# Optimization experiments

Measured on AMD Instinct MI355X. Metric: run time of the kernel, lower is better.

## Reference

```python
import jax, jax.numpy as jnp
import numpy as np

D = 512; H = 8; DH = D // H; DFF = 4 * D; INNER = 2 * D; K = 31
B = 8; S = 1024
EPS = 1e-5


def layer_norm(x, g, b):
    m = jnp.mean(x, axis=-1, keepdims=True)
    v = jnp.mean(jnp.square(x - m), axis=-1, keepdims=True)
    return (x - m) * jax.lax.rsqrt(v + EPS) * g + b


def setup_inputs() -> dict:
    key = jax.random.key(0)
    ks = iter(jax.random.split(key, 32))
    w = lambda *s: jax.random.normal(next(ks), s, dtype=jnp.float32) * 0.02
    d = {
        "x": jax.random.normal(next(ks), (B, S, D), dtype=jnp.float32),
        # FF module 1
        "ln1_g": jnp.ones((D,)), "ln1_b": jnp.zeros((D,)),
        "ff1_w1": w(DFF, D), "ff1_b1": jnp.zeros((DFF,)),
        "ff1_w2": w(D, DFF), "ff1_b2": jnp.zeros((D,)),
        # attention
        "lna_g": jnp.ones((D,)), "lna_b": jnp.zeros((D,)),
        "qkv_w": w(3 * D, D), "qkv_b": jnp.zeros((3 * D,)),
        "out_w": w(D, D), "out_b": jnp.zeros((D,)),
        # conv module
        "lnc_g": jnp.ones((D,)), "lnc_b": jnp.zeros((D,)),
        "pw1_w": w(INNER, D), "pw1_b": jnp.zeros((INNER,)),
        "dw_w": w(D, 1, K), "dw_b": jnp.zeros((D,)),
        "bn_g": jnp.ones((D,)), "bn_b": jnp.zeros((D,)),
        "bn_mean": jnp.zeros((D,)), "bn_var": jnp.ones((D,)),
        "pw2_w": w(D, D), "pw2_b": jnp.zeros((D,)),
        # FF module 2
        "ln2_g": jnp.ones((D,)), "ln2_b": jnp.zeros((D,)),
        "ff2_w1": w(DFF, D), "ff2_b1": jnp.zeros((DFF,)),
        "ff2_w2": w(D, DFF), "ff2_b2": jnp.zeros((D,)),
        # final layer norm
        "lnf_g": jnp.ones((D,)), "lnf_b": jnp.zeros((D,)),
    }
    return d


def _ff(x, g, b, w1, b1, w2, b2):
    h = layer_norm(x, g, b)
    h = jax.nn.silu(h @ w1.T + b1)
    h = h @ w2.T + b2
    return h + x  # FeedForwardModule adds its own residual


def _attn(x, g, b, qkv_w, qkv_b, out_w, out_b):
    h = layer_norm(x, g, b)
    qkv = (h @ qkv_w.T + qkv_b).reshape(B, S, 3, H, DH)
    q, k, v = qkv[:, :, 0], qkv[:, :, 1], qkv[:, :, 2]  # [B,S,H,DH]
    scores = jnp.einsum('bqhd,bkhd->bhqk', q, k) / np.sqrt(DH).astype(np.float32)
    probs = jax.nn.softmax(scores, axis=-1)
    ctx = jnp.einsum('bhqk,bkhd->bqhd', probs, v).reshape(B, S, D)
    return ctx @ out_w.T + out_b


def _conv(x, g, b, pw1_w, pw1_b, dw_w, dw_b, bn_g, bn_b, bn_mean, bn_var, pw2_w, pw2_b):
    h = layer_norm(x, g, b)
    y = h @ pw1_w.T + pw1_b                      # [B,S,2D] pointwise conv1
    a, gate = jnp.split(y, 2, axis=-1)           # GLU along channel dim
    y = a * jax.nn.sigmoid(gate)                 # [B,S,D]
    y = y.transpose(0, 2, 1)                     # [B,D,S]
    y = jax.lax.conv_general_dilated(
        y, dw_w, window_strides=(1,), padding=((K // 2, K // 2),),
        dimension_numbers=('NCH', 'OIH', 'NCH'), feature_group_count=D)
    y = y + dw_b[None, :, None]
    y = (y - bn_mean[None, :, None]) * jax.lax.rsqrt(bn_var + EPS)[None, :, None]
    y = y * bn_g[None, :, None] + bn_b[None, :, None]
    y = jax.nn.silu(y)
    y = y.transpose(0, 2, 1)                     # [B,S,D]
    y = y @ pw2_w.T + pw2_b
    return y + x  # ConvModule adds its own residual


def reference(x, ln1_g, ln1_b, ff1_w1, ff1_b1, ff1_w2, ff1_b2,
              lna_g, lna_b, qkv_w, qkv_b, out_w, out_b,
              lnc_g, lnc_b, pw1_w, pw1_b, dw_w, dw_b,
              bn_g, bn_b, bn_mean, bn_var, pw2_w, pw2_b,
              ln2_g, ln2_b, ff2_w1, ff2_b1, ff2_w2, ff2_b2,
              lnf_g, lnf_b):
    x = x + 0.5 * _ff(x, ln1_g, ln1_b, ff1_w1, ff1_b1, ff1_w2, ff1_b2)
    x = x + _attn(x, lna_g, lna_b, qkv_w, qkv_b, out_w, out_b)
    x = x + _conv(x, lnc_g, lnc_b, pw1_w, pw1_b, dw_w, dw_b,
                  bn_g, bn_b, bn_mean, bn_var, pw2_w, pw2_b)
    x = x + 0.5 * _ff(x, ln2_g, ln2_b, ff2_w1, ff2_b1, ff2_w2, ff2_b2)
    return layer_norm(x, lnf_g, lnf_b)
```

## Files before the change

kernel.cpp:

```cpp
#include <hip/hip_runtime.h>
#include <hip/hip_bf16.h>

typedef __attribute__((ext_vector_type(8))) short bf16x8;
typedef __attribute__((ext_vector_type(4))) float f32x4;

#define NTOK 8192
#define SEQ  1024
#define NH   8

__device__ __forceinline__ float bfs2f(short s) {
  union { unsigned u; float f; } x; x.u = ((unsigned)(unsigned short)s) << 16; return x.f;
}
__device__ __forceinline__ short f2bfs(float f) {
  __hip_bfloat16 h = __float2bfloat16(f);
  return *reinterpret_cast<short*>(&h);
}
__device__ __forceinline__ float bfp2f(const __hip_bfloat16* p) {
  return bfs2f(*reinterpret_cast<const short*>(p));
}

__device__ __forceinline__ void gld16(const void* g, void* l) {
  __builtin_amdgcn_global_load_lds(
      (__attribute__((address_space(1))) void*)const_cast<void*>(g),
      (__attribute__((address_space(3))) void*)l, 16, 0, 0);
}

struct WSeg { const float* src; unsigned dst_off; unsigned nvec; };
struct WPack { WSeg s[8]; };

__global__ __launch_bounds__(256) void cast_wall_kernel(WPack p,
                                                        __hip_bfloat16* __restrict__ dst) {
  unsigned v = blockIdx.x * 256 + threadIdx.x;
#pragma unroll
  for (int t = 0; t < 8; ++t) {
    if (v < p.s[t].nvec) {
      const float* s = p.s[t].src + (size_t)v * 8;
      f32x4 a = *reinterpret_cast<const f32x4*>(s);
      f32x4 b = *reinterpret_cast<const f32x4*>(s + 4);
      bf16x8 o;
#pragma unroll
      for (int j = 0; j < 4; ++j) { o[j] = f2bfs(a[j]); o[4 + j] = f2bfs(b[j]); }
      *reinterpret_cast<bf16x8*>(reinterpret_cast<short*>(dst) +
                                 (size_t)(p.s[t].dst_off + v) * 8) = o;
      return;
    }
    v -= p.s[t].nvec;
  }
}

__global__ __launch_bounds__(256) void cast_dww_kernel(const float* __restrict__ src,
                                                       __hip_bfloat16* __restrict__ dst) {
  for (int k = 0; k < 31; ++k)
    for (int c = threadIdx.x; c < 512; c += 256)
      dst[k * 512 + c] = __float2bfloat16(src[c * 31 + k]);
}

struct PtrPack { const void* p[23]; };

__global__ __launch_bounds__(256) void cast_small_kernel(PtrPack pk,
                                                         __hip_bfloat16* __restrict__ dst) {
  constexpr int sizes[23] = {512, 512, 2048, 512, 512, 512, 1536, 512, 512, 512, 1024, 512,
                             512, 512, 512, 512, 512, 512, 512, 2048, 512, 512, 512};
  int off = 0;
  for (int t = 0; t < 23; ++t) {
    const int n = sizes[t];
    for (int i = threadIdx.x; i < n; i += 256)
      dst[off + i] = __float2bfloat16(((const float*)pk.p[t])[i]);
    off += n;
  }
}

__global__ void ws_bad_kernel(float* __restrict__ out) {
  if (threadIdx.x == 0) out[0] = 5000.f;
}

__global__ __launch_bounds__(256) void ln_kernel(const float* __restrict__ in,
                                                 const __hip_bfloat16* __restrict__ g,
                                                 const __hip_bfloat16* __restrict__ b,
                                                 __hip_bfloat16* __restrict__ out) {
  const int wv = threadIdx.x >> 6, ln = threadIdx.x & 63;
  const int row = blockIdx.x * 4 + wv;
  const float* p = in + (size_t)row * 512 + ln * 8;
  float v[8];
  {
    const f32x4* p4 = reinterpret_cast<const f32x4*>(p);
    f32x4 a = p4[0], c = p4[1];
#pragma unroll
    for (int j = 0; j < 4; ++j) { v[j] = a[j]; v[4 + j] = c[j]; }
  }
  float s = 0.f;
#pragma unroll
  for (int j = 0; j < 8; ++j) s += v[j];
  for (int m = 1; m < 64; m <<= 1) s += __shfl_xor(s, m);
  const float mean = s * (1.f / 512.f);
  float q = 0.f;
#pragma unroll
  for (int j = 0; j < 8; ++j) { float d = v[j] - mean; q += d * d; }
  for (int m = 1; m < 64; m <<= 1) q += __shfl_xor(q, m);
  const float rstd = rsqrtf(q * (1.f / 512.f) + 1e-5f);
  bf16x8 gg = *reinterpret_cast<const bf16x8*>(g + ln * 8);
  bf16x8 bb = *reinterpret_cast<const bf16x8*>(b + ln * 8);
  bf16x8 ov;
#pragma unroll
  for (int j = 0; j < 8; ++j)
    ov[j] = f2bfs((v[j] - mean) * rstd * bfs2f(gg[j]) + bfs2f(bb[j]));
  *reinterpret_cast<bf16x8*>(out + (size_t)row * 512 + ln * 8) = ov;
}

__global__ __launch_bounds__(256) void lnf_kernel(const float* __restrict__ in,
                                                  const __hip_bfloat16* __restrict__ g,
                                                  const __hip_bfloat16* __restrict__ b,
                                                  float* __restrict__ out) {
  const int wv = threadIdx.x >> 6, ln = threadIdx.x & 63;
  const int row = blockIdx.x * 4 + wv;
  const float* p = in + (size_t)row * 512 + ln * 8;
  float v[8];
  {
    const f32x4* p4 = reinterpret_cast<const f32x4*>(p);
    f32x4 a = p4[0], c = p4[1];
#pragma unroll
    for (int j = 0; j < 4; ++j) { v[j] = a[j]; v[4 + j] = c[j]; }
  }
  float s = 0.f;
#pragma unroll
  for (int j = 0; j < 8; ++j) s += v[j];
  for (int m = 1; m < 64; m <<= 1) s += __shfl_xor(s, m);
  const float mean = s * (1.f / 512.f);
  float q = 0.f;
#pragma unroll
  for (int j = 0; j < 8; ++j) { float d = v[j] - mean; q += d * d; }
  for (int m = 1; m < 64; m <<= 1) q += __shfl_xor(q, m);
  const float rstd = rsqrtf(q * (1.f / 512.f) + 1e-5f);
  bf16x8 gg = *reinterpret_cast<const bf16x8*>(g + ln * 8);
  bf16x8 bb = *reinterpret_cast<const bf16x8*>(b + ln * 8);
  f32x4 o0, o1;
#pragma unroll
  for (int j = 0; j < 4; ++j) {
    o0[j] = (v[j] - mean) * rstd * bfs2f(gg[j]) + bfs2f(bb[j]);
    o1[j] = (v[4 + j] - mean) * rstd * bfs2f(gg[4 + j]) + bfs2f(bb[4 + j]);
  }
  float* op = out + (size_t)row * 512 + ln * 8;
  *reinterpret_cast<f32x4*>(op) = o0;
  *reinterpret_cast<f32x4*>(op + 4) = o1;
}

template <int EPI>
__global__ __launch_bounds__(256, 3) void gemm_bt(const __hip_bfloat16* __restrict__ A,
                                                  const __hip_bfloat16* __restrict__ W,
                                                  const __hip_bfloat16* __restrict__ bias,
                                                  __hip_bfloat16* __restrict__ outb,
                                                  float* __restrict__ resid,
                                                  int K, int M, float alpha, float beta) {
  __shared__ __align__(16) __hip_bfloat16 As[128 * 64];
  __shared__ __align__(16) __hip_bfloat16 Bs[128 * 64];
  const int tid = threadIdx.x;
  const int wv = tid >> 6, ln = tid & 63;
  const int hi = ln >> 4, lo = ln & 15;
  const int lo7 = lo & 7;
  const int gx = gridDim.x;
  const int nwg = gx * gridDim.y;
  const int t = blockIdx.y * gx + blockIdx.x;
  const int w = (t & 7) * (nwg >> 3) + (t >> 3);
  const int n0 = (w & (gx - 1)) * 128;
  const int m0 = (w / gx) * 128;
  const int wr = wv >> 1, wc = wv & 1;
  const int srow = ln >> 3;
  const int scolz = (((ln & 7) ^ srow) << 3);

  f32x4 acc[4][4] = {};

  for (int k0 = 0; k0 < K; k0 += 64) {
    __syncthreads();
#pragma unroll
    for (int i = 0; i < 4; ++i) {
      const int grp = i * 4 + wv;
      const int row = grp * 8 + srow;
      gld16(A + (size_t)(n0 + row) * K + k0 + scolz, As + grp * 512);
      gld16(W + (size_t)(m0 + row) * K + k0 + scolz, Bs + grp * 512);
    }
    __syncthreads();
#pragma unroll
    for (int kk2 = 0; kk2 < 2; ++kk2) {
      const int g0 = ((kk2 * 4 + hi) ^ lo7) << 3;
      bf16x8 af[4], bfr[4];
#pragma unroll
      for (int r = 0; r < 4; ++r)
        af[r] = *reinterpret_cast<const bf16x8*>(As + (wr * 64 + r * 16 + lo) * 64 + g0);
#pragma unroll
      for (int c = 0; c < 4; ++c)
        bfr[c] = *reinterpret_cast<const bf16x8*>(Bs + (wc * 64 + c * 16 + lo) * 64 + g0);
#pragma unroll
      for (int r = 0; r < 4; ++r)
#pragma unroll
        for (int c = 0; c < 4; ++c)
          acc[r][c] = __builtin_amdgcn_mfma_f32_16x16x32_bf16(af[r], bfr[c], acc[r][c], 0, 0, 0);
    }
  }

#pragma unroll
  for (int r = 0; r < 4; ++r) {
#pragma unroll
    for (int c = 0; c < 4; ++c) {
      const int m = m0 + wc * 64 + c * 16 + lo;
      const float bv = bfp2f(bias + m);
#pragma unroll
      for (int j = 0; j < 4; ++j) {
        const int n = n0 + wr * 64 + r * 16 + hi * 4 + j;
        float v = acc[r][c][j] + bv;
        if constexpr (EPI == 1) v = v / (1.f + __expf(-v));
        if constexpr (EPI <= 1) {
          outb[(size_t)n * M + m] = __float2bfloat16(v);
        } else {
          const size_t idx = (size_t)n * 512 + m;
          resid[idx] = alpha * resid[idx] + beta * v;
        }
      }
    }
  }
}

__global__ __launch_bounds__(256, 4) void gemm64_resid(const __hip_bfloat16* __restrict__ A,
                                                       const __hip_bfloat16* __restrict__ W,
                                                       const __hip_bfloat16* __restrict__ bias,
                                                       const float* __restrict__ rsrc,
                                                       float* __restrict__ resid,
                                                       int K, float alpha, float beta) {
  __shared__ __align__(16) __hip_bfloat16 As[64 * 64];
  __shared__ __align__(16) __hip_bfloat16 Bs[128 * 64];
  const int tid = threadIdx.x;
  const int wv = tid >> 6, ln = tid & 63;
  const int hi = ln >> 4, lo = ln & 15;
  const int lo7 = lo & 7;
  const int gx = gridDim.x;
  const int nwg = gx * gridDim.y;
  const int t = blockIdx.y * gx + blockIdx.x;
  const int w = (t & 7) * (nwg >> 3) + (t >> 3);
  const int n0 = (w & (gx - 1)) * 64;
  const int m0 = (w / gx) * 128;
  const int wr = wv >> 1, wc = wv & 1;
  const int srow = ln >> 3;
  const int scolz = (((ln & 7) ^ srow) << 3);

  f32x4 acc[2][4] = {};

  for (int k0 = 0; k0 < K; k0 += 64) {
    __syncthreads();
#pragma unroll
    for (int i = 0; i < 2; ++i) {
      const int grp = i * 4 + wv;
      gld16(A + (size_t)(n0 + grp * 8 + srow) * K + k0 + scolz, As + grp * 512);
    }
#pragma unroll
    for (int i = 0; i < 4; ++i) {
      const int grp = i * 4 + wv;
      gld16(W + (size_t)(m0 + grp * 8 + srow) * K + k0 + scolz, Bs + grp * 512);
    }
    __syncthreads();
#pragma unroll
    for (int kk2 = 0; kk2 < 2; ++kk2) {
      const int g0 = ((kk2 * 4 + hi) ^ lo7) << 3;
      bf16x8 af[2], bfr[4];
#pragma unroll
      for (int r = 0; r < 2; ++r)
        af[r] = *reinterpret_cast<const bf16x8*>(As + (wr * 32 + r * 16 + lo) * 64 + g0);
#pragma unroll
      for (int c = 0; c < 4; ++c)
        bfr[c] = *reinterpret_cast<const bf16x8*>(Bs + (wc * 64 + c * 16 + lo) * 64 + g0);
#pragma unroll
      for (int r = 0; r < 2; ++r)
#pragma unroll
        for (int c = 0; c < 4; ++c)
          acc[r][c] = __builtin_amdgcn_mfma_f32_16x16x32_bf16(af[r], bfr[c], acc[r][c], 0, 0, 0);
    }
  }

#pragma unroll
  for (int r = 0; r < 2; ++r) {
#pragma unroll
    for (int c = 0; c < 4; ++c) {
      const int m = m0 + wc * 64 + c * 16 + lo;
      const float bv = bfp2f(bias + m);
#pragma unroll
      for (int j = 0; j < 4; ++j) {
        const int n = n0 + wr * 32 + r * 16 + hi * 4 + j;
        const size_t idx = (size_t)n * 512 + m;
        resid[idx] = alpha * rsrc[idx] + beta * (acc[r][c][j] + bv);
      }
    }
  }
}

__global__ __launch_bounds__(256) void vtrans_kernel(const __hip_bfloat16* __restrict__ qkv,
                                                     __hip_bfloat16* __restrict__ vT) {
  __shared__ __hip_bfloat16 tile[64][65];
  const int bh = blockIdx.x;
  const int s0 = blockIdx.y * 64;
  const int b = bh >> 3, h = bh & 7;
  const int c = threadIdx.x & 63;
  const int r4 = threadIdx.x >> 6;
#pragma unroll
  for (int i = 0; i < 16; ++i) {
    const int s = r4 * 16 + i;
    tile[s][c] = qkv[(size_t)(b * 1024 + s0 + s) * 1536 + 1024 + h * 64 + c];
  }
  __syncthreads();
#pragma unroll
  for (int i = 0; i < 16; ++i) {
    const int d = r4 * 16 + i;
    vT[((size_t)bh * 64 + d) * 1024 + s0 + c] = tile[c][d];
  }
}

__global__ __launch_bounds__(256, 2) void attn_kernel(const __hip_bfloat16* __restrict__ qkv,
                                                      const __hip_bfloat16* __restrict__ vT,
                                                      __hip_bfloat16* __restrict__ ctx) {
  __shared__ __align__(16) short Ks[2][64 * 64];
  __shared__ __align__(16) short Vs[2][64 * 64];
  __shared__ __align__(16) short P[4][16][64];
  const int tid = threadIdx.x;
  const int wv = tid >> 6, ln = tid & 63;
  const int hi = ln >> 4, lo = ln & 15;
  const int lo7 = lo & 7;
  const int blk = ((blockIdx.x & 7) << 6) | (blockIdx.x >> 3);
  const int qt = blk & 7, h = (blk >> 3) & 7, b = blk >> 6;
  const int q0 = qt * 128 + wv * 16;

  const int srow8 = ln >> 3;
  const int gsrc = (ln & 7) ^ srow8;

  bf16x8 aq0a, aq1a, aq0b, aq1b;
  {
    const __hip_bfloat16* qpa = qkv + (size_t)(b * SEQ + q0 + lo) * 1536 + h * 64 + hi * 8;
    const __hip_bfloat16* qpb = qpa + (size_t)64 * 1536;
    bf16x8 r0 = *reinterpret_cast<const bf16x8*>(qpa);
    bf16x8 r1 = *reinterpret_cast<const bf16x8*>(qpa + 32);
    bf16x8 r2 = *reinterpret_cast<const bf16x8*>(qpb);
    bf16x8 r3 = *reinterpret_cast<const bf16x8*>(qpb + 32);
#pragma unroll
    for (int j = 0; j < 8; ++j) {
      aq0a[j] = f2bfs(bfs2f(r0[j]) * 0.125f);
      aq1a[j] = f2bfs(bfs2f(r1[j]) * 0.125f);
      aq0b[j] = f2bfs(bfs2f(r2[j]) * 0.125f);
      aq1b[j] = f2bfs(bfs2f(r3[j]) * 0.125f);
    }
  }

  const __hip_bfloat16* kbase = qkv + 512 + h * 64 + (size_t)b * SEQ * 1536;
  const __hip_bfloat16* vbase = vT + (size_t)(b * NH + h) * 64 * 1024;

  f32x4 oaccA[4] = {}, oaccB[4] = {};
  float lrowA[4] = {0.f, 0.f, 0.f, 0.f};
  float lrowB[4] = {0.f, 0.f, 0.f, 0.f};

#pragma unroll
  for (int c = 0; c < 2; ++c) {
    const int r = c * 32 + wv * 8 + srow8;
    gld16(kbase + (size_t)r * 1536 + gsrc * 8, &Ks[0][(c * 32 + wv * 8) * 64]);
    gld16(vbase + (size_t)r * 1024 + gsrc * 8, &Vs[0][(c * 32 + wv * 8) * 64]);
  }
  __syncthreads();

  int cb = 0;
  for (int kt = 0; kt < 16; ++kt) {
    if (kt < 15) {
      const int kb2 = (kt + 1) * 64;
#pragma unroll
      for (int c = 0; c < 2; ++c) {
        const int r = c * 32 + wv * 8 + srow8;
        gld16(kbase + (size_t)(kb2 + r) * 1536 + gsrc * 8,
              &Ks[cb ^ 1][(c * 32 + wv * 8) * 64]);
        gld16(vbase + (size_t)r * 1024 + kb2 + gsrc * 8,
              &Vs[cb ^ 1][(c * 32 + wv * 8) * 64]);
      }
    }

    bf16x8 bk0[4], bk1[4];
#pragma unroll
    for (int nt = 0; nt < 4; ++nt) {
      const short* kr = &Ks[cb][(nt * 16 + lo) * 64];
      bk0[nt] = *reinterpret_cast<const bf16x8*>(kr + ((hi ^ lo7) << 3));
      bk1[nt] = *reinterpret_cast<const bf16x8*>(kr + (((hi + 4) ^ lo7) << 3));
    }
    f32x4 scA[4] = {}, scB[4] = {};
#pragma unroll
    for (int nt = 0; nt < 4; ++nt) {
      scA[nt] = __builtin_amdgcn_mfma_f32_16x16x32_bf16(aq0a, bk0[nt], scA[nt], 0, 0, 0);
      scA[nt] = __builtin_amdgcn_mfma_f32_16x16x32_bf16(aq1a, bk1[nt], scA[nt], 0, 0, 0);
      scB[nt] = __builtin_amdgcn_mfma_f32_16x16x32_bf16(aq0b, bk0[nt], scB[nt], 0, 0, 0);
      scB[nt] = __builtin_amdgcn_mfma_f32_16x16x32_bf16(aq1b, bk1[nt], scB[nt], 0, 0, 0);
    }

    bf16x8 bv0[4], bv1[4];
#pragma unroll
    for (int dt = 0; dt < 4; ++dt) {
      const short* vr = &Vs[cb][(dt * 16 + lo) * 64];
      bv0[dt] = *reinterpret_cast<const bf16x8*>(vr + ((hi ^ lo7) << 3));
      bv1[dt] = *reinterpret_cast<const bf16x8*>(vr + (((hi + 4) ^ lo7) << 3));
    }

#pragma unroll
    for (int j = 0; j < 4; ++j) {
      const int prow = hi * 4 + j;
      const int pswz = (prow & 7) << 3;
#pragma unroll
      for (int nt = 0; nt < 4; ++nt) {
        const float p = __expf(scA[nt][j]);
        P[wv][prow][(nt * 16 + lo) ^ pswz] = f2bfs(p);
        lrowA[j] += p;
      }
    }
    asm volatile("" ::: "memory");
    {
      const short* pr = &P[wv][lo][0];
      bf16x8 ap0 = *reinterpret_cast<const bf16x8*>(pr + ((hi ^ lo7) << 3));
      bf16x8 ap1 = *reinterpret_cast<const bf16x8*>(pr + (((hi + 4) ^ lo7) << 3));
#pragma unroll
      for (int dt = 0; dt < 4; ++dt) {
        oaccA[dt] = __builtin_amdgcn_mfma_f32_16x16x32_bf16(ap0, bv0[dt], oaccA[dt], 0, 0, 0);
        oaccA[dt] = __builtin_amdgcn_mfma_f32_16x16x32_bf16(ap1, bv1[dt], oaccA[dt], 0, 0, 0);
      }
    }
    asm volatile("" ::: "memory");

#pragma unroll
    for (int j = 0; j < 4; ++j) {
      const int prow = hi * 4 + j;
      const int pswz = (prow & 7) << 3;
#pragma unroll
      for (int nt = 0; nt < 4; ++nt) {
        const float p = __expf(scB[nt][j]);
        P[wv][prow][(nt * 16 + lo) ^ pswz] = f2bfs(p);
        lrowB[j] += p;
      }
    }
    asm volatile("" ::: "memory");
    {
      const short* pr = &P[wv][lo][0];
      bf16x8 ap0 = *reinterpret_cast<const bf16x8*>(pr + ((hi ^ lo7) << 3));
      bf16x8 ap1 = *reinterpret_cast<const bf16x8*>(pr + (((hi + 4) ^ lo7) << 3));
#pragma unroll
      for (int dt = 0; dt < 4; ++dt) {
        oaccB[dt] = __builtin_amdgcn_mfma_f32_16x16x32_bf16(ap0, bv0[dt], oaccB[dt], 0, 0, 0);
        oaccB[dt] = __builtin_amdgcn_mfma_f32_16x16x32_bf16(ap1, bv1[dt], oaccB[dt], 0, 0, 0);
      }
    }
    __syncthreads();
    cb ^= 1;
  }

#pragma unroll
  for (int j = 0; j < 4; ++j) {
    float sa = lrowA[j], sb = lrowB[j];
    sa += __shfl_xor(sa, 1); sb += __shfl_xor(sb, 1);
    sa += __shfl_xor(sa, 2); sb += __shfl_xor(sb, 2);
    sa += __shfl_xor(sa, 4); sb += __shfl_xor(sb, 4);
    sa += __shfl_xor(sa, 8); sb += __shfl_xor(sb, 8);
    lrowA[j] = sa; lrowB[j] = sb;
  }

#pragma unroll
  for (int dt = 0; dt < 4; ++dt)
#pragma unroll
    for (int j = 0; j < 4; ++j) {
      const int d = h * 64 + dt * 16 + lo;
      const int na = b * SEQ + q0 + hi * 4 + j;
      ctx[(size_t)na * 512 + d] = __float2bfloat16(oaccA[dt][j] / lrowA[j]);
      const int nb = na + 64;
      ctx[(size_t)nb * 512 + d] = __float2bfloat16(oaccB[dt][j] / lrowB[j]);
    }
}

__global__ __launch_bounds__(256) void glu8_kernel(const __hip_bfloat16* __restrict__ y,
                                                   __hip_bfloat16* __restrict__ o) {
  const int i = blockIdx.x * 256 + threadIdx.x;
  const int c8 = i & 63;
  const int n = i >> 6;
  const short* yp = reinterpret_cast<const short*>(y) + (size_t)n * 1024 + c8 * 8;
  bf16x8 a = *reinterpret_cast<const bf16x8*>(yp);
  bf16x8 g = *reinterpret_cast<const bf16x8*>(yp + 512);
  bf16x8 ov;
#pragma unroll
  for (int j = 0; j < 8; ++j) {
    const float av = bfs2f(a[j]);
    const float gv = bfs2f(g[j]);
    ov[j] = f2bfs(av / (1.f + __expf(-gv)));
  }
  *reinterpret_cast<bf16x8*>(reinterpret_cast<short*>(o) + (size_t)n * 512 + c8 * 8) = ov;
}

__global__ __launch_bounds__(256) void dwconv8_kernel(const __hip_bfloat16* __restrict__ cin,
                                                      const __hip_bfloat16* __restrict__ wkT,
                                                      const __hip_bfloat16* __restrict__ cb,
                                                      const __hip_bfloat16* __restrict__ bng,
                                                      const __hip_bfloat16* __restrict__ bnb,
                                                      const __hip_bfloat16* __restrict__ bnm,
                                                      const __hip_bfloat16* __restrict__ bnv,
                                                      __hip_bfloat16* __restrict__ outp) {
  const int i = blockIdx.x * 256 + threadIdx.x;
  const int c8 = i & 63;
  const int n = i >> 6;
  const int t = n & 1023;
  const int base = n - t;
  const int co = c8 * 8;

  float acc[8];
  {
    bf16x8 bv = *reinterpret_cast<const bf16x8*>(cb + co);
#pragma unroll
    for (int j = 0; j < 8; ++j) acc[j] = bfs2f(bv[j]);
  }
  const int k0 = (t >= 15) ? 0 : (15 - t);
  const int k1 = (t <= SEQ - 16) ? 31 : (SEQ - 1 - t + 16);
  const short* cin_s = reinterpret_cast<const short*>(cin);
  const short* wk_s = reinterpret_cast<const short*>(wkT);
  for (int k = k0; k < k1; ++k) {
    const int ts = t + k - 15;
    bf16x8 xv = *reinterpret_cast<const bf16x8*>(cin_s + (((size_t)(base + ts)) << 9) + co);
    bf16x8 wv = *reinterpret_cast<const bf16x8*>(wk_s + k * 512 + co);
#pragma unroll
    for (int j = 0; j < 8; ++j) acc[j] += bfs2f(xv[j]) * bfs2f(wv[j]);
  }
  bf16x8 g = *reinterpret_cast<const bf16x8*>(bng + co);
  bf16x8 bb = *reinterpret_cast<const bf16x8*>(bnb + co);
  bf16x8 bm = *reinterpret_cast<const bf16x8*>(bnm + co);
  bf16x8 bvv = *reinterpret_cast<const bf16x8*>(bnv + co);
  bf16x8 ov;
#pragma unroll
  for (int j = 0; j < 8; ++j) {
    const float scl = bfs2f(g[j]) * rsqrtf(bfs2f(bvv[j]) + 1e-5f);
    float v = (acc[j] - bfs2f(bm[j])) * scl + bfs2f(bb[j]);
    v = v / (1.f + __expf(-v));
    ov[j] = f2bfs(v);
  }
  *reinterpret_cast<bf16x8*>(reinterpret_cast<short*>(outp) + ((size_t)n << 9) + co) = ov;
}

extern "C" void kernel_launch(void* const* d_in, const int* in_sizes, int n_in,
                              void* d_out, int out_size, void* d_ws, size_t ws_size,
                              hipStream_t stream) {
  float* out = (float*)d_out;
  if (ws_size < ((size_t)80 << 20)) {
    ws_bad_kernel<<<1, 64, 0, stream>>>(out);
    return;
  }

  const float* x = (const float*)d_in[0];

  char* ws = (char*)d_ws;
  float*          xs = (float*)ws;
  __hip_bfloat16* t0 = (__hip_bfloat16*)(ws + ((size_t)16 << 20));
  __hip_bfloat16* t1 = (__hip_bfloat16*)(ws + ((size_t)24 << 20));
  __hip_bfloat16* t2 = (__hip_bfloat16*)(ws + ((size_t)56 << 20));
  __hip_bfloat16* wc = (__hip_bfloat16*)(ws + ((size_t)64 << 20));
  __hip_bfloat16* vT = t1 + (size_t)NTOK * 1536;

  __hip_bfloat16* wc_ff1_w1 = wc + 0;
  __hip_bfloat16* wc_ff1_w2 = wc + 1048576;
  __hip_bfloat16* wc_qkv_w  = wc + 2097152;
  __hip_bfloat16* wc_out_w  = wc + 2883584;
  __hip_bfloat16* wc_pw1_w  = wc + 3145728;
  __hip_bfloat16* wc_pw2_w  = wc + 3670016;
  __hip_bfloat16* wc_ff2_w1 = wc + 3932160;
  __hip_bfloat16* wc_ff2_w2 = wc + 4980736;
  __hip_bfloat16* wc_dwT    = wc + 6029312;
  __hip_bfloat16* sm        = wc + 6045184;
  __hip_bfloat16* c_ln1_g = sm + 0,     *c_ln1_b = sm + 512,   *c_ff1_b1 = sm + 1024;
  __hip_bfloat16* c_ff1_b2 = sm + 3072, *c_lna_g = sm + 3584,  *c_lna_b = sm + 4096;
  __hip_bfloat16* c_qkv_b = sm + 4608,  *c_out_b = sm + 6144,  *c_lnc_g = sm + 6656;
  __hip_bfloat16* c_lnc_b = sm + 7168,  *c_pw1_b = sm + 7680,  *c_dw_b = sm + 8704;
  __hip_bfloat16* c_bn_g = sm + 9216,   *c_bn_b = sm + 9728,   *c_bn_m = sm + 10240;
  __hip_bfloat16* c_bn_v = sm + 10752,  *c_pw2_b = sm + 11264, *c_ln2_g = sm + 11776;
  __hip_bfloat16* c_ln2_b = sm + 12288, *c_ff2_b1 = sm + 12800, *c_ff2_b2 = sm + 14848;
  __hip_bfloat16* c_lnf_g = sm + 15360, *c_lnf_b = sm + 15872;

  {
    WPack wp;
    wp.s[0] = {(const float*)d_in[3],  0,      131072};
    wp.s[1] = {(const float*)d_in[5],  131072, 131072};
    wp.s[2] = {(const float*)d_in[9],  262144, 98304};
    wp.s[3] = {(const float*)d_in[11], 360448, 32768};
    wp.s[4] = {(const float*)d_in[15], 393216, 65536};
    wp.s[5] = {(const float*)d_in[23], 458752, 32768};
    wp.s[6] = {(const float*)d_in[27], 491520, 131072};
    wp.s[7] = {(const float*)d_in[29], 622592, 131072};
    cast_wall_kernel<<<2944, 256, 0, stream>>>(wp, wc);
  }
  cast_dww_kernel<<<1, 256, 0, stream>>>((const float*)d_in[17], wc_dwT);
  PtrPack pk;
  const int small_idx[23] = {1, 2, 4, 6, 7, 8, 10, 12, 13, 14, 16, 18,
                             19, 20, 21, 22, 24, 25, 26, 28, 30, 31, 32};
  for (int t = 0; t < 23; ++t) pk.p[t] = d_in[small_idx[t]];
  cast_small_kernel<<<1, 256, 0, stream>>>(pk, sm);

  ln_kernel<<<2048, 256, 0, stream>>>(x, c_ln1_g, c_ln1_b, t0);
  gemm_bt<1><<<dim3(64, 16), 256, 0, stream>>>(t0, wc_ff1_w1, c_ff1_b1, t1, nullptr, 512, 2048, 0.f, 0.f);
  gemm64_resid<<<dim3(128, 4), 256, 0, stream>>>(t1, wc_ff1_w2, c_ff1_b2, x, xs, 2048, 1.5f, 0.5f);

  ln_kernel<<<2048, 256, 0, stream>>>(xs, c_lna_g, c_lna_b, t0);
  gemm_bt<0><<<dim3(64, 12), 256, 0, stream>>>(t0, wc_qkv_w, c_qkv_b, t1, nullptr, 512, 1536, 0.f, 0.f);
  vtrans_kernel<<<dim3(64, 16), 256, 0, stream>>>(t1, vT);
  attn_kernel<<<512, 256, 0, stream>>>(t1, vT, t2);
  gemm64_resid<<<dim3(128, 4), 256, 0, stream>>>(t2, wc_out_w, c_out_b, xs, xs, 512, 1.0f, 1.0f);

  ln_kernel<<<2048, 256, 0, stream>>>(xs, c_lnc_g, c_lnc_b, t0);
  gemm_bt<0><<<dim3(64, 8), 256, 0, stream>>>(t0, wc_pw1_w, c_pw1_b, t1, nullptr, 512, 1024, 0.f, 0.f);
  glu8_kernel<<<2048, 256, 0, stream>>>(t1, t2);
  dwconv8_kernel<<<2048, 256, 0, stream>>>(t2, wc_dwT, c_dw_b, c_bn_g, c_bn_b, c_bn_m, c_bn_v, t0);
  gemm64_resid<<<dim3(128, 4), 256, 0, stream>>>(t0, wc_pw2_w, c_pw2_b, xs, xs, 512, 2.0f, 1.0f);

  ln_kernel<<<2048, 256, 0, stream>>>(xs, c_ln2_g, c_ln2_b, t0);
  gemm_bt<1><<<dim3(64, 16), 256, 0, stream>>>(t0, wc_ff2_w1, c_ff2_b1, t1, nullptr, 512, 2048, 0.f, 0.f);
  gemm64_resid<<<dim3(128, 4), 256, 0, stream>>>(t1, wc_ff2_w2, c_ff2_b2, xs, xs, 2048, 1.5f, 0.5f);

  lnf_kernel<<<2048, 256, 0, stream>>>(xs, c_lnf_g, c_lnf_b, out);
}
```

Baseline: 303.3 us.

## Fuse V transpose into QKV GEMM epilogue and keep depthwise conv in fp32

The QKV GEMM gets a new epilogue (EPI==3) that writes the V columns straight into the transposed vT layout as 4-element bf16 vectors, which removes the separate vtrans kernel and its extra read and write of V. Separately, the GLU output and the depthwise conv weights are now stored in fp32 instead of bf16, and the conv loads fp32 vectors. This looks like a precision change that doubles the conv's input traffic. The fused epilogue also writes 8-byte strided stores instead of going through a shared-memory transpose.

New measurement: 319.1 us. +5.2%, slower.

```diff
diff --git a/kernel.cpp b/kernel.cpp
--- a/kernel.cpp
+++ b/kernel.cpp
@@ -2,6 +2,7 @@
 #include <hip/hip_bf16.h>
 
 typedef __attribute__((ext_vector_type(8))) short bf16x8;
+typedef __attribute__((ext_vector_type(4))) short bf16x4;
 typedef __attribute__((ext_vector_type(4))) float f32x4;
 
 #define NTOK 8192
@@ -48,11 +49,11 @@
   }
 }
 
-__global__ __launch_bounds__(256) void cast_dww_kernel(const float* __restrict__ src,
-                                                       __hip_bfloat16* __restrict__ dst) {
+__global__ __launch_bounds__(256) void cast_dwwf_kernel(const float* __restrict__ src,
+                                                        float* __restrict__ dst) {
   for (int k = 0; k < 31; ++k)
     for (int c = threadIdx.x; c < 512; c += 256)
-      dst[k * 512 + c] = __float2bfloat16(src[c * 31 + k]);
+      dst[k * 512 + c] = src[c * 31 + k];
 }
 
 struct PtrPack { const void* p[23]; };
@@ -150,6 +151,7 @@
                                                   const __hip_bfloat16* __restrict__ bias,
                                                   __hip_bfloat16* __restrict__ outb,
                                                   float* __restrict__ resid,
+                                                  __hip_bfloat16* __restrict__ vTout,
                                                   int K, int M, float alpha, float beta) {
   __shared__ __align__(16) __hip_bfloat16 As[128 * 64];
   __shared__ __align__(16) __hip_bfloat16 Bs[128 * 64];
@@ -203,16 +205,29 @@
     for (int c = 0; c < 4; ++c) {
       const int m = m0 + wc * 64 + c * 16 + lo;
       const float bv = bfp2f(bias + m);
+      const int nb = n0 + wr * 64 + r * 16 + hi * 4;
+      if constexpr (EPI == 3) {
+        if (m >= 1024) {
+          const int hd = m - 1024;
+          __hip_bfloat16* vp = vTout +
+              ((size_t)((nb >> 10) * NH + (hd >> 6)) * 64 + (hd & 63)) * 1024 + (nb & 1023);
+          bf16x4 vv;
+#pragma unroll
+          for (int j = 0; j < 4; ++j) vv[j] = f2bfs(acc[r][c][j] + bv);
+          *reinterpret_cast<bf16x4*>(vp) = vv;
+          continue;
+        }
+      }
 #pragma unroll
       for (int j = 0; j < 4; ++j) {
-        const int n = n0 + wr * 64 + r * 16 + hi * 4 + j;
+        const int n = nb + j;
         float v = acc[r][c][j] + bv;
         if constexpr (EPI == 1) v = v / (1.f + __expf(-v));
-        if constexpr (EPI <= 1) {
-          outb[(size_t)n * M + m] = __float2bfloat16(v);
-        } else {
+        if constexpr (EPI == 2) {
           const size_t idx = (size_t)n * 512 + m;
           resid[idx] = alpha * resid[idx] + beta * v;
+        } else {
+          outb[(size_t)n * M + m] = __float2bfloat16(v);
         }
       }
     }
@@ -290,27 +305,6 @@
   }
 }
 
-__global__ __launch_bounds__(256) void vtrans_kernel(const __hip_bfloat16* __restrict__ qkv,
-                                                     __hip_bfloat16* __restrict__ vT) {
-  __shared__ __hip_bfloat16 tile[64][65];
-  const int bh = blockIdx.x;
-  const int s0 = blockIdx.y * 64;
-  const int b = bh >> 3, h = bh & 7;
-  const int c = threadIdx.x & 63;
-  const int r4 = threadIdx.x >> 6;
-#pragma unroll
-  for (int i = 0; i < 16; ++i) {
-    const int s = r4 * 16 + i;
-    tile[s][c] = qkv[(size_t)(b * 1024 + s0 + s) * 1536 + 1024 + h * 64 + c];
-  }
-  __syncthreads();
-#pragma unroll
-  for (int i = 0; i < 16; ++i) {
-    const int d = r4 * 16 + i;
-    vT[((size_t)bh * 64 + d) * 1024 + s0 + c] = tile[c][d];
-  }
-}
-
 __global__ __launch_bounds__(256, 2) void attn_kernel(const __hip_bfloat16* __restrict__ qkv,
                                                       const __hip_bfloat16* __restrict__ vT,
                                                       __hip_bfloat16* __restrict__ ctx) {
@@ -470,32 +464,35 @@
     }
 }
 
-__global__ __launch_bounds__(256) void glu8_kernel(const __hip_bfloat16* __restrict__ y,
-                                                   __hip_bfloat16* __restrict__ o) {
+__global__ __launch_bounds__(256) void glu8f_kernel(const __hip_bfloat16* __restrict__ y,
+                                                    float* __restrict__ o) {
   const int i = blockIdx.x * 256 + threadIdx.x;
   const int c8 = i & 63;
   const int n = i >> 6;
   const short* yp = reinterpret_cast<const short*>(y) + (size_t)n * 1024 + c8 * 8;
   bf16x8 a = *reinterpret_cast<const bf16x8*>(yp);
   bf16x8 g = *reinterpret_cast<const bf16x8*>(yp + 512);
-  bf16x8 ov;
-#pragma unroll
-  for (int j = 0; j < 8; ++j) {
-    const float av = bfs2f(a[j]);
-    const float gv = bfs2f(g[j]);
-    ov[j] = f2bfs(av / (1.f + __expf(-gv)));
-  }
-  *reinterpret_cast<bf16x8*>(reinterpret_cast<short*>(o) + (size_t)n * 512 + c8 * 8) = ov;
-}
-
-__global__ __launch_bounds__(256) void dwconv8_kernel(const __hip_bfloat16* __restrict__ cin,
-                                                      const __hip_bfloat16* __restrict__ wkT,
-                                                      const __hip_bfloat16* __restrict__ cb,
-                                                      const __hip_bfloat16* __restrict__ bng,
-                                                      const __hip_bfloat16* __restrict__ bnb,
-                                                      const __hip_bfloat16* __restrict__ bnm,
-                                                      const __hip_bfloat16* __restrict__ bnv,
-                                                      __hip_bfloat16* __restrict__ outp) {
+  f32x4 o0, o1;
+#pragma unroll
+  for (int j = 0; j < 4; ++j) {
+    const float a0 = bfs2f(a[j]), g0 = bfs2f(g[j]);
+    const float a1 = bfs2f(a[4 + j]), g1 = bfs2f(g[4 + j]);
+    o0[j] = a0 / (1.f + __expf(-g0));
+    o1[j] = a1 / (1.f + __expf(-g1));
+  }
+  float* op = o + (size_t)n * 512 + c8 * 8;
+  *reinterpret_cast<f32x4*>(op) = o0;
+  *reinterpret_cast<f32x4*>(op + 4) = o1;
+}
+
+__global__ __launch_bounds__(256) void dwconv8f_kernel(const float* __restrict__ cin,
+                                                       const float* __restrict__ wkT,
+                                                       const __hip_bfloat16* __restrict__ cb,
+                                                       const __hip_bfloat16* __restrict__ bng,
+                                                       const __hip_bfloat16* __restrict__ bnb,
+                                                       const __hip_bfloat16* __restrict__ bnm,
+                                                       const __hip_bfloat16* __restrict__ bnv,
+                                                       __hip_bfloat16* __restrict__ outp) {
   const int i = blockIdx.x * 256 + threadIdx.x;
   const int c8 = i & 63;
   const int n = i >> 6;
@@ -511,14 +508,19 @@
   }
   const int k0 = (t >= 15) ? 0 : (15 - t);
   const int k1 = (t <= SEQ - 16) ? 31 : (SEQ - 1 - t + 16);
-  const short* cin_s = reinterpret_cast<const short*>(cin);
-  const short* wk_s = reinterpret_cast<const short*>(wkT);
   for (int k = k0; k < k1; ++k) {
     const int ts = t + k - 15;
-    bf16x8 xv = *reinterpret_cast<const bf16x8*>(cin_s + (((size_t)(base + ts)) << 9) + co);
-    bf16x8 wv = *reinterpret_cast<const bf16x8*>(wk_s + k * 512 + co);
-#pragma unroll
-    for (int j = 0; j < 8; ++j) acc[j] += bfs2f(xv[j]) * bfs2f(wv[j]);
+    const float* xp = cin + (((size_t)(base + ts)) << 9) + co;
+    const float* wp = wkT + k * 512 + co;
+    f32x4 x0 = *reinterpret_cast<const f32x4*>(xp);
+    f32x4 x1 = *reinterpret_cast<const f32x4*>(xp + 4);
+    f32x4 w0 = *reinterpret_cast<const f32x4*>(wp);
+    f32x4 w1 = *reinterpret_cast<const f32x4*>(wp + 4);
+#pragma unroll
+    for (int j = 0; j < 4; ++j) {
+      acc[j] += x0[j] * w0[j];
+      acc[4 + j] += x1[j] * w1[j];
+    }
   }
   bf16x8 g = *reinterpret_cast<const bf16x8*>(bng + co);
   bf16x8 bb = *reinterpret_cast<const bf16x8*>(bnb + co);
@@ -547,12 +549,14 @@
   const float* x = (const float*)d_in[0];
 
   char* ws = (char*)d_ws;
-  float*          xs = (float*)ws;
-  __hip_bfloat16* t0 = (__hip_bfloat16*)(ws + ((size_t)16 << 20));
-  __hip_bfloat16* t1 = (__hip_bfloat16*)(ws + ((size_t)24 << 20));
-  __hip_bfloat16* t2 = (__hip_bfloat16*)(ws + ((size_t)56 << 20));
-  __hip_bfloat16* wc = (__hip_bfloat16*)(ws + ((size_t)64 << 20));
-  __hip_bfloat16* vT = t1 + (size_t)NTOK * 1536;
+  float*          xs  = (float*)ws;
+  __hip_bfloat16* t0  = (__hip_bfloat16*)(ws + ((size_t)16 << 20));
+  __hip_bfloat16* t1  = (__hip_bfloat16*)(ws + ((size_t)24 << 20));
+  float*          t2f = (float*)(ws + ((size_t)40 << 20));
+  __hip_bfloat16* t2  = (__hip_bfloat16*)(ws + ((size_t)56 << 20));
+  __hip_bfloat16* wc  = (__hip_bfloat16*)(ws + ((size_t)64 << 20));
+  float*          dwTf = (float*)(ws + ((size_t)78 << 20));
+  __hip_bfloat16* vT  = t1 + (size_t)NTOK * 1536;
 
   __hip_bfloat16* wc_ff1_w1 = wc + 0;
   __hip_bfloat16* wc_ff1_w2 = wc + 1048576;
@@ -562,7 +566,6 @@
   __hip_bfloat16* wc_pw2_w  = wc + 3670016;
   __hip_bfloat16* wc_ff2_w1 = wc + 3932160;
   __hip_bfloat16* wc_ff2_w2 = wc + 4980736;
-  __hip_bfloat16* wc_dwT    = wc + 6029312;
   __hip_bfloat16* sm        = wc + 6045184;
   __hip_bfloat16* c_ln1_g = sm + 0,     *c_ln1_b = sm + 512,   *c_ff1_b1 = sm + 1024;
   __hip_bfloat16* c_ff1_b2 = sm + 3072, *c_lna_g = sm + 3584,  *c_lna_b = sm + 4096;
@@ -585,7 +588,7 @@
     wp.s[7] = {(const float*)d_in[29], 622592, 131072};
     cast_wall_kernel<<<2944, 256, 0, stream>>>(wp, wc);
   }
-  cast_dww_kernel<<<1, 256, 0, stream>>>((const float*)d_in[17], wc_dwT);
+  cast_dwwf_kernel<<<1, 256, 0, stream>>>((const float*)d_in[17], dwTf);
   PtrPack pk;
   const int small_idx[23] = {1, 2, 4, 6, 7, 8, 10, 12, 13, 14, 16, 18,
                              19, 20, 21, 22, 24, 25, 26, 28, 30, 31, 32};
@@ -593,23 +596,22 @@
   cast_small_kernel<<<1, 256, 0, stream>>>(pk, sm);
 
   ln_kernel<<<2048, 256, 0, stream>>>(x, c_ln1_g, c_ln1_b, t0);
-  gemm_bt<1><<<dim3(64, 16), 256, 0, stream>>>(t0, wc_ff1_w1, c_ff1_b1, t1, nullptr, 512, 2048, 0.f, 0.f);
+  gemm_bt<1><<<dim3(64, 16), 256, 0, stream>>>(t0, wc_ff1_w1, c_ff1_b1, t1, nullptr, nullptr, 512, 2048, 0.f, 0.f);
   gemm64_resid<<<dim3(128, 4), 256, 0, stream>>>(t1, wc_ff1_w2, c_ff1_b2, x, xs, 2048, 1.5f, 0.5f);
 
   ln_kernel<<<2048, 256, 0, stream>>>(xs, c_lna_g, c_lna_b, t0);
-  gemm_bt<0><<<dim3(64, 12), 256, 0, stream>>>(t0, wc_qkv_w, c_qkv_b, t1, nullptr, 512, 1536, 0.f, 0.f);
-  vtrans_kernel<<<dim3(64, 16), 256, 0, stream>>>(t1, vT);
+  gemm_bt<3><<<dim3(64, 12), 256, 0, stream>>>(t0, wc_qkv_w, c_qkv_b, t1, nullptr, vT, 512, 1536, 0.f, 0.f);
   attn_kernel<<<512, 256, 0, stream>>>(t1, vT, t2);
   gemm64_resid<<<dim3(128, 4), 256, 0, stream>>>(t2, wc_out_w, c_out_b, xs, xs, 512, 1.0f, 1.0f);
 
   ln_kernel<<<2048, 256, 0, stream>>>(xs, c_lnc_g, c_lnc_b, t0);
-  gemm_bt<0><<<dim3(64, 8), 256, 0, stream>>>(t0, wc_pw1_w, c_pw1_b, t1, nullptr, 512, 1024, 0.f, 0.f);
-  glu8_kernel<<<2048, 256, 0, stream>>>(t1, t2);
-  dwconv8_kernel<<<2048, 256, 0, stream>>>(t2, wc_dwT, c_dw_b, c_bn_g, c_bn_b, c_bn_m, c_bn_v, t0);
+  gemm_bt<0><<<dim3(64, 8), 256, 0, stream>>>(t0, wc_pw1_w, c_pw1_b, t1, nullptr, nullptr, 512, 1024, 0.f, 0.f);
+  glu8f_kernel<<<2048, 256, 0, stream>>>(t1, t2f);
+  dwconv8f_kernel<<<2048, 256, 0, stream>>>(t2f, dwTf, c_dw_b, c_bn_g, c_bn_b, c_bn_m, c_bn_v, t0);
   gemm64_resid<<<dim3(128, 4), 256, 0, stream>>>(t0, wc_pw2_w, c_pw2_b, xs, xs, 512, 2.0f, 1.0f);
 
   ln_kernel<<<2048, 256, 0, stream>>>(xs, c_ln2_g, c_ln2_b, t0);
-  gemm_bt<1><<<dim3(64, 16), 256, 0, stream>>>(t0, wc_ff2_w1, c_ff2_b1, t1, nullptr, 512, 2048, 0.f, 0.f);
+  gemm_bt<1><<<dim3(64, 16), 256, 0, stream>>>(t0, wc_ff2_w1, c_ff2_b1, t1, nullptr, nullptr, 512, 2048, 0.f, 0.f);
   gemm64_resid<<<dim3(128, 4), 256, 0, stream>>>(t1, wc_ff2_w2, c_ff2_b2, xs, xs, 2048, 1.5f, 0.5f);
 
   lnf_kernel<<<2048, 256, 0, stream>>>(xs, c_lnf_g, c_lnf_b, out);
```
